# Optimization experiments

Measured on AMD Instinct MI355X. Metric: run time of the kernel, lower is better.

## Reference

```python
import jax, jax.numpy as jnp
import numpy as np

B, T, D, H = 2, 4096, 512, 8
HD = D // H

def setup_inputs() -> dict:
    key = jax.random.key(0)
    ks = jax.random.split(key, 5)
    x = jax.random.normal(ks[0], (B, T, D), dtype=jnp.float32)
    # causal mask: masked_fill where mask == 0
    mask = jnp.tril(jnp.ones((T, T), dtype=jnp.int32))[None, None, :, :]
    qkv_w = jax.random.normal(ks[1], (D, 3 * D), dtype=jnp.float32) * (D ** -0.5)
    qkv_b = jax.random.normal(ks[2], (3 * D,), dtype=jnp.float32) * 0.02
    proj_w = jax.random.normal(ks[3], (D, D), dtype=jnp.float32) * (D ** -0.5)
    proj_b = jax.random.normal(ks[4], (D,), dtype=jnp.float32) * 0.02
    return {"x": x, "mask": mask, "qkv_w": qkv_w, "qkv_b": qkv_b,
            "proj_w": proj_w, "proj_b": proj_b}

def reference(x, mask, qkv_w, qkv_b, proj_w, proj_b):
    b, t, c = x.shape
    qkv = x @ qkv_w + qkv_b                      # [B,T,3D]
    q, k, v = jnp.split(qkv, 3, axis=-1)
    # [B,T,D] -> [B,H,T,hd]
    def heads(a):
        return a.reshape(b, t, H, HD).transpose(0, 2, 1, 3)
    q, k, v = heads(q), heads(k), heads(v)
    att = jnp.einsum('bhqd,bhkd->bhqk', q, k) / (HD ** 0.5)
    att = jnp.where(mask == 0, -jnp.inf, att)
    att = jax.nn.softmax(att, axis=-1)           # dropout p=0.0 -> identity
    out = jnp.einsum('bhqk,bhkd->bhqd', att, v)  # [B,H,T,hd]
    out = out.transpose(0, 2, 1, 3).reshape(b, t, c)
    return out @ proj_w + proj_b
```

## Files before the change

### kernel.cpp

```cpp
#include <hip/hip_runtime.h>
#include <hip/hip_bf16.h>


typedef __attribute__((ext_vector_type(8))) short bf16x8;
typedef __attribute__((ext_vector_type(4))) float f32x4;
typedef __attribute__((ext_vector_type(16))) float f32x16;
typedef __attribute__((ext_vector_type(2))) int i32x2;

#define DEV static __device__ __forceinline__

DEV unsigned short f2bf(float f) {
    union { float f; unsigned u; } a; a.f = f;
    unsigned r = a.u + 0x7FFFu + ((a.u >> 16) & 1u);
    return (unsigned short)(r >> 16);
}

DEV unsigned pack2(float a, float b) {
    unsigned r;
    asm("v_cvt_pk_bf16_f32 %0, %1, %2" : "=v"(r) : "v"(a), "v"(b));
    return r;
}

DEV void glds16(const void* g, void* l) {
    __builtin_amdgcn_global_load_lds(
        (const __attribute__((address_space(1))) void*)g,
        (__attribute__((address_space(3))) void*)l,
        16, 0, 0);
}

DEV f32x4 mfma(bf16x8 a, bf16x8 b, f32x4 c) {
    return __builtin_amdgcn_mfma_f32_16x16x32_bf16(a, b, c, 0, 0, 0);
}

DEV f32x16 mfma32(bf16x8 a, bf16x8 b, f32x16 c) {
    return __builtin_amdgcn_mfma_f32_32x32x16_bf16(a, b, c, 0, 0, 0);
}

DEV void plswap(unsigned& a, unsigned& b) {
#if __has_builtin(__builtin_amdgcn_permlane32_swap)
    i32x2 r = __builtin_amdgcn_permlane32_swap((int)a, (int)b, false, false);
    a = (unsigned)r.x; b = (unsigned)r.y;
#else
    unsigned sa = __shfl_xor(a, 32), sb = __shfl_xor(b, 32);
    bool hi = (threadIdx.x & 32) != 0;
    unsigned na = hi ? sb : a;
    unsigned nb = hi ? b : sa;
    a = na; b = nb;
#endif
}

DEV float xhalf_sum(float x) {
    unsigned a = __float_as_uint(x), b = a;
    plswap(a, b);
    return __uint_as_float(a) + __uint_as_float(b);
}

__global__ __launch_bounds__(256) void k_cast(const float* __restrict__ x,
                                              unsigned short* __restrict__ xb, int n4) {
    for (int i = blockIdx.x * 256 + threadIdx.x; i < n4; i += gridDim.x * 256) {
        float4 v = ((const float4*)x)[i];
        ushort4 o;
        o.x = f2bf(v.x); o.y = f2bf(v.y); o.z = f2bf(v.z); o.w = f2bf(v.w);
        ((ushort4*)xb)[i] = o;
    }
}

__global__ __launch_bounds__(256) void k_tcast2(const float* __restrict__ qkv_w,
                                                unsigned short* __restrict__ wqkvT,
                                                const float* __restrict__ proj_w,
                                                unsigned short* __restrict__ wprojT) {
    __shared__ float t[64][65];
    const int tid = threadIdx.x;
    int id = blockIdx.x;
    const float* src; unsigned short* dst; int R, C, bx, by;
    if (id < 192) { src = qkv_w; dst = wqkvT; R = 512; C = 1536; bx = id % 24; by = id / 24; }
    else { id -= 192; src = proj_w; dst = wprojT; R = 512; C = 512; bx = id & 7; by = id >> 3; }
#pragma unroll
    for (int e = 0; e < 16; ++e) {
        int idx = e * 256 + tid;
        int r = idx >> 6, c = idx & 63;
        t[r][c] = src[(by * 64 + r) * C + bx * 64 + c];
    }
    __syncthreads();
#pragma unroll
    for (int e = 0; e < 16; ++e) {
        int idx = e * 256 + tid;
        int r = idx >> 6, c = idx & 63;
        dst[(bx * 64 + r) * R + by * 64 + c] = f2bf(t[c][r]);
    }
}

__global__ __launch_bounds__(256) void k_gemm_qkv(
    const unsigned short* __restrict__ xb, const unsigned short* __restrict__ wT,
    const float* __restrict__ bias,
    unsigned short* __restrict__ Qb, unsigned short* __restrict__ Kb,
    unsigned short* __restrict__ Vtb)
{
    __shared__ __attribute__((aligned(16))) unsigned short lA[128 * 64];
    __shared__ __attribute__((aligned(16))) unsigned short lB[128 * 64];
    const int tid = threadIdx.x, lane = tid & 63, w = tid >> 6;
    const int qi = lane & 15, g = lane >> 4;
    const int bm = blockIdx.x & 63, bn = blockIdx.x >> 6;
    const int m0 = bm * 128, n0 = bn * 128;
    const int wr = w >> 1, wc = w & 1;
    const int srow = lane >> 3, sch = (lane & 7) ^ srow;
    const int swz = (qi & 7) << 4;
    f32x4 zero = {0.f, 0.f, 0.f, 0.f};
    f32x4 acc[4][4];
#pragma unroll
    for (int i = 0; i < 4; ++i)
#pragma unroll
        for (int j = 0; j < 4; ++j) acc[i][j] = zero;

    for (int kt = 0; kt < 8; ++kt) {
#pragma unroll
        for (int i = 0; i < 4; ++i) {
            int c = w * 4 + i;
            int row = c * 8 + srow;
            glds16(xb + (m0 + row) * 512 + kt * 64 + sch * 8, (char*)lA + c * 1024);
            glds16(wT + (n0 + row) * 512 + kt * 64 + sch * 8, (char*)lB + c * 1024);
        }
        __syncthreads();
#pragma unroll
        for (int k2 = 0; k2 < 2; ++k2) {
            bf16x8 af[4], bfr[4];
#pragma unroll
            for (int i = 0; i < 4; ++i) {
                int ra = wr * 64 + i * 16 + qi;
                af[i] = *(const bf16x8*)((const char*)lA + ra * 128 + ((k2 * 64 + g * 16) ^ swz));
                int rb = wc * 64 + i * 16 + qi;
                bfr[i] = *(const bf16x8*)((const char*)lB + rb * 128 + ((k2 * 64 + g * 16) ^ swz));
            }
#pragma unroll
            for (int mi = 0; mi < 4; ++mi)
#pragma unroll
                for (int ni = 0; ni < 4; ++ni)
                    acc[mi][ni] = mfma(af[mi], bfr[ni], acc[mi][ni]);
        }
        __syncthreads();
    }

    const int comp = n0 >> 9;
#pragma unroll
    for (int mi = 0; mi < 4; ++mi) {
        int mbase = m0 + wr * 64 + mi * 16 + g * 4;
        int b = mbase >> 12, t = mbase & 4095;
#pragma unroll
        for (int ni = 0; ni < 4; ++ni) {
            int n = n0 + wc * 64 + ni * 16 + qi;
            float bn = bias[n];
            int nn = n & 511;
            int h = nn >> 6, d = nn & 63;
            if (comp == 0) {
                unsigned short* dst = Qb + ((b * 8 + h) * 4096 + t) * 64 + d;
#pragma unroll
                for (int r = 0; r < 4; ++r)
                    dst[r * 64] = f2bf((acc[mi][ni][r] + bn) * 0.18033688011112042f);
            } else if (comp == 1) {
                unsigned short* dst = Kb + ((b * 8 + h) * 4096 + t) * 64 + d;
#pragma unroll
                for (int r = 0; r < 4; ++r)
                    dst[r * 64] = f2bf(acc[mi][ni][r] + bn);
            } else {
                ushort4 pk4;
                pk4.x = f2bf(acc[mi][ni][0] + bn);
                pk4.y = f2bf(acc[mi][ni][1] + bn);
                pk4.z = f2bf(acc[mi][ni][2] + bn);
                pk4.w = f2bf(acc[mi][ni][3] + bn);
                *(ushort4*)(Vtb + ((b * 8 + h) * 64 + d) * 4096 + t) = pk4;
            }
        }
    }
}

__global__ __launch_bounds__(512) void k_attn(
    const unsigned short* __restrict__ Qb, const unsigned short* __restrict__ Kb,
    const unsigned short* __restrict__ Vtb, unsigned short* __restrict__ Ob)
{
    __shared__ __attribute__((aligned(16))) char smem[65536];
    const int tid = threadIdx.x, lane = tid & 63, w = tid >> 6;
    const int l31 = lane & 31, l7 = lane & 7, h = lane >> 5;
    const int pr = w >> 1, sub = w & 1;
    const int idx = blockIdx.x;
    const int bh = idx & 15;
    const int p = idx >> 4;
    const unsigned short* Qh = Qb + bh * 4096 * 64;
    const unsigned short* Kh = Kb + bh * 4096 * 64;
    const unsigned short* Vh = Vtb + bh * 4096 * 64;
    const float NEGINF = -__builtin_inff();

    char* myK = smem + pr * 16384;
    char* myV = myK + 8192;

    const int srw = lane >> 3;
    const int sxor = (l7 ^ srw) * 8;
    const int kOffE = (sub * 32 + srw) * 64 + sxor;
    const int vOffE = (sub * 32 + srw) * 4096 + sxor;
    const int ldsO = sub * 4096;

    const int rowbase = l31 * 128;
    int cx[4];
#pragma unroll
    for (int c = 0; c < 4; ++c) cx[c] = ((2 * c + h) ^ l7) * 16;

    const int qrel = (sub << 5) + l31;

    f32x16 z16;
#pragma unroll
    for (int r = 0; r < 16; ++r) z16[r] = 0.f;

    for (int si = 0; si < 2; ++si) {
        const int qt = si ? p : 63 - p;
        const int Tmax = (qt >> 2) + 1;
        const int qrow = qt * 64 + sub * 32 + l31;

        bf16x8 qf[4];
#pragma unroll
        for (int c = 0; c < 4; ++c)
            qf[c] = *(const bf16x8*)(Qh + qrow * 64 + 16 * c + 8 * h);

        f32x16 o0 = z16, o1 = z16;
        float li = 0.f;

        for (int t = 0; t < Tmax; ++t) {
            const int j = 4 * t + pr;
            const bool act = (j <= qt);
            if (act) {
                const unsigned short* kp = Kh + j * 4096 + kOffE;
                const unsigned short* vp = Vh + vOffE + j * 64;
#pragma unroll
                for (int i = 0; i < 4; ++i) {
                    glds16(kp + i * 512,   myK + ldsO + i * 1024);
                    glds16(vp + i * 32768, myV + ldsO + i * 1024);
                }
            }
            __syncthreads();
            if (act) {
                const char* lk = myK;
                const char* lv = myV;
                f32x16 s0, s1;
                __builtin_amdgcn_s_setprio(1);
                {
                    bf16x8 k0 = *(const bf16x8*)(lk + rowbase + cx[0]);
                    bf16x8 k1 = *(const bf16x8*)(lk + 4096 + rowbase + cx[0]);
                    s0 = mfma32(k0, qf[0], z16);
                    s1 = mfma32(k1, qf[0], z16);
                }
#pragma unroll
                for (int c = 1; c < 4; ++c) {
                    bf16x8 k0 = *(const bf16x8*)(lk + rowbase + cx[c]);
                    bf16x8 k1 = *(const bf16x8*)(lk + 4096 + rowbase + cx[c]);
                    s0 = mfma32(k0, qf[c], s0);
                    s1 = mfma32(k1, qf[c], s1);
                }
                __builtin_amdgcn_s_setprio(0);

                if (j == qt) {
#pragma unroll
                    for (int r = 0; r < 16; ++r) {
                        int rr = 4 * h + (r & 3) + 8 * (r >> 2);
                        if (rr > qrel) s0[r] = NEGINF;
                        if (rr + 32 > qrel) s1[r] = NEGINF;
                    }
                }

#pragma unroll
                for (int r = 0; r < 16; ++r) {
                    s0[r] = __builtin_amdgcn_exp2f(s0[r]);
                    s1[r] = __builtin_amdgcn_exp2f(s1[r]);
                }
                float a8[8];
#pragma unroll
                for (int r = 0; r < 8; ++r)
                    a8[r] = (s0[r] + s0[r + 8]) + (s1[r] + s1[r + 8]);
                float b0 = (a8[0] + a8[4]) + (a8[1] + a8[5]);
                float b1 = (a8[2] + a8[6]) + (a8[3] + a8[7]);
                li += xhalf_sum(b0 + b1);

                __builtin_amdgcn_s_setprio(1);
#pragma unroll
                for (int c2 = 0; c2 < 4; ++c2) {
                    unsigned u0w, u1w, u2w, u3w;
                    if (c2 < 2) {
                        const int b0i = 8 * c2;
                        u0w = pack2(s0[b0i + 0], s0[b0i + 1]);
                        u1w = pack2(s0[b0i + 2], s0[b0i + 3]);
                        u2w = pack2(s0[b0i + 4], s0[b0i + 5]);
                        u3w = pack2(s0[b0i + 6], s0[b0i + 7]);
                    } else {
                        const int b0i = 8 * (c2 - 2);
                        u0w = pack2(s1[b0i + 0], s1[b0i + 1]);
                        u1w = pack2(s1[b0i + 2], s1[b0i + 3]);
                        u2w = pack2(s1[b0i + 4], s1[b0i + 5]);
                        u3w = pack2(s1[b0i + 6], s1[b0i + 7]);
                    }
                    plswap(u0w, u2w);
                    plswap(u1w, u3w);
                    union { unsigned u[4]; bf16x8 v; } pf;
                    pf.u[0] = u0w; pf.u[1] = u1w; pf.u[2] = u2w; pf.u[3] = u3w;
                    bf16x8 v0 = *(const bf16x8*)(lv + rowbase + cx[c2]);
                    bf16x8 v1 = *(const bf16x8*)(lv + 4096 + rowbase + cx[c2]);
                    o0 = mfma32(v0, pf.v, o0);
                    o1 = mfma32(v1, pf.v, o1);
                }
                __builtin_amdgcn_s_setprio(0);
            }
            __syncthreads();
        }

        float* fsm = (float*)smem;
        if (pr != 0) {
            float* slot = fsm + ((((pr - 1) << 1) + sub) * 64 + lane) * 36;
#pragma unroll
            for (int r4 = 0; r4 < 4; ++r4) {
                f32x4 v0 = {o0[4 * r4], o0[4 * r4 + 1], o0[4 * r4 + 2], o0[4 * r4 + 3]};
                f32x4 v1 = {o1[4 * r4], o1[4 * r4 + 1], o1[4 * r4 + 2], o1[4 * r4 + 3]};
                *(f32x4*)(slot + 4 * r4) = v0;
                *(f32x4*)(slot + 16 + 4 * r4) = v1;
            }
            slot[32] = li;
        }
        __syncthreads();
        if (pr == 0) {
            float l = li;
#pragma unroll
            for (int i = 0; i < 3; ++i) {
                const float* s = fsm + (((i << 1) + sub) * 64 + lane) * 36;
                l += s[32];
#pragma unroll
                for (int r4 = 0; r4 < 4; ++r4) {
                    f32x4 a = *(const f32x4*)(s + 4 * r4);
                    f32x4 b = *(const f32x4*)(s + 16 + 4 * r4);
#pragma unroll
                    for (int e = 0; e < 4; ++e) {
                        o0[4 * r4 + e] += a[e];
                        o1[4 * r4 + e] += b[e];
                    }
                }
            }
            float inv = 1.f / l;
            unsigned short* orow = Ob + ((bh >> 3) * 4096 + qrow) * 512 + (bh & 7) * 64 + 4 * h;
#pragma unroll
            for (int g2 = 0; g2 < 4; ++g2) {
                union { ushort4 s4; unsigned u[2]; } a;
                a.u[0] = pack2(o0[4 * g2 + 0] * inv, o0[4 * g2 + 1] * inv);
                a.u[1] = pack2(o0[4 * g2 + 2] * inv, o0[4 * g2 + 3] * inv);
                *(ushort4*)(orow + 8 * g2) = a.s4;
                a.u[0] = pack2(o1[4 * g2 + 0] * inv, o1[4 * g2 + 1] * inv);
                a.u[1] = pack2(o1[4 * g2 + 2] * inv, o1[4 * g2 + 3] * inv);
                *(ushort4*)(orow + 32 + 8 * g2) = a.s4;
            }
        }
        __syncthreads();
    }
}

__global__ __launch_bounds__(256) void k_gemm_proj(
    const unsigned short* __restrict__ Ob, const unsigned short* __restrict__ wT,
    const float* __restrict__ bias, float* __restrict__ out)
{
    __shared__ __attribute__((aligned(16))) unsigned short lA[128 * 64];
    __shared__ __attribute__((aligned(16))) unsigned short lB[128 * 64];
    const int tid = threadIdx.x, lane = tid & 63, w = tid >> 6;
    const int qi = lane & 15, g = lane >> 4;
    const int bm = blockIdx.x & 63, bn = blockIdx.x >> 6;
    const int m0 = bm * 128, n0 = bn * 128;
    const int wr = w >> 1, wc = w & 1;
    const int srow = lane >> 3, sch = (lane & 7) ^ srow;
    const int swz = (qi & 7) << 4;
    f32x4 zero = {0.f, 0.f, 0.f, 0.f};
    f32x4 acc[4][4];
#pragma unroll
    for (int i = 0; i < 4; ++i)
#pragma unroll
        for (int j = 0; j < 4; ++j) acc[i][j] = zero;

    for (int kt = 0; kt < 8; ++kt) {
#pragma unroll
        for (int i = 0; i < 4; ++i) {
            int c = w * 4 + i;
            int row = c * 8 + srow;
            glds16(Ob + (m0 + row) * 512 + kt * 64 + sch * 8, (char*)lA + c * 1024);
            glds16(wT + (n0 + row) * 512 + kt * 64 + sch * 8, (char*)lB + c * 1024);
        }
        __syncthreads();
#pragma unroll
        for (int k2 = 0; k2 < 2; ++k2) {
            bf16x8 af[4], bfr[4];
#pragma unroll
            for (int i = 0; i < 4; ++i) {
                int ra = wr * 64 + i * 16 + qi;
                af[i] = *(const bf16x8*)((const char*)lA + ra * 128 + ((k2 * 64 + g * 16) ^ swz));
                int rb = wc * 64 + i * 16 + qi;
                bfr[i] = *(const bf16x8*)((const char*)lB + rb * 128 + ((k2 * 64 + g * 16) ^ swz));
            }
#pragma unroll
            for (int mi = 0; mi < 4; ++mi)
#pragma unroll
                for (int ni = 0; ni < 4; ++ni)
                    acc[mi][ni] = mfma(af[mi], bfr[ni], acc[mi][ni]);
        }
        __syncthreads();
    }

#pragma unroll
    for (int mi = 0; mi < 4; ++mi) {
        int mbase = m0 + wr * 64 + mi * 16 + g * 4;
#pragma unroll
        for (int ni = 0; ni < 4; ++ni) {
            int n = n0 + wc * 64 + ni * 16 + qi;
            float bn = bias[n];
#pragma unroll
            for (int r = 0; r < 4; ++r)
                out[(mbase + r) * 512 + n] = acc[mi][ni][r] + bn;
        }
    }
}

extern "C" void kernel_launch(void* const* d_in, const int* in_sizes, int n_in,
                              void* d_out, int out_size, void* d_ws, size_t ws_size,
                              hipStream_t stream) {
    const float* x      = (const float*)d_in[0];
    const float* qkv_w  = (const float*)d_in[2];
    const float* qkv_b  = (const float*)d_in[3];
    const float* proj_w = (const float*)d_in[4];
    const float* proj_b = (const float*)d_in[5];

    char* ws = (char*)d_ws;
    unsigned short* xb     = (unsigned short*)(ws);
    unsigned short* wqkvT  = (unsigned short*)(ws +  8388608);
    unsigned short* wprojT = (unsigned short*)(ws +  9961472);
    unsigned short* Qb     = (unsigned short*)(ws + 10485760);
    unsigned short* Kb     = (unsigned short*)(ws + 18874368);
    unsigned short* Vtb    = (unsigned short*)(ws + 27262976);
    unsigned short* Ob     = (unsigned short*)(ws + 35651584);
    float* out = (float*)d_out;

    k_cast<<<2048, 256, 0, stream>>>(x, xb, 8192 * 512 / 4);
    k_tcast2<<<256, 256, 0, stream>>>(qkv_w, wqkvT, proj_w, wprojT);
    k_gemm_qkv<<<768, 256, 0, stream>>>(xb, wqkvT, qkv_b, Qb, Kb, Vtb);
    k_attn<<<512, 512, 0, stream>>>(Qb, Kb, Vtb, Ob);
    k_gemm_proj<<<256, 256, 0, stream>>>(Ob, wprojT, proj_b, out);
}
```

Measured before the change: 102.8 us.

## Double-buffer K/V tiles in LDS to prefetch the next tile during compute

Shared memory for the attention kernel doubles to 128KB so each wave pair has two K/V buffers. The next key tile is issued with global_load_lds before the current one is computed, and a partial vmcnt wait lets the loads overlap the MFMA work. The intent is to hide global-to-LDS latency that the single-buffer loop exposed at every barrier. The cost is double the LDS per block, which can limit occupancy to one block per CU, and correctness now depends on hand-written waitcnt and barrier ordering.

```diff
diff --git a/kernel.cpp b/kernel.cpp
--- a/kernel.cpp
+++ b/kernel.cpp
@@ -177,7 +177,7 @@
     const unsigned short* __restrict__ Qb, const unsigned short* __restrict__ Kb,
     const unsigned short* __restrict__ Vtb, unsigned short* __restrict__ Ob)
 {
-    __shared__ __attribute__((aligned(16))) char smem[65536];
+    __shared__ __attribute__((aligned(16))) char smem[131072];
     const int tid = threadIdx.x, lane = tid & 63, w = tid >> 6;
     const int l31 = lane & 31, l7 = lane & 7, h = lane >> 5;
     const int pr = w >> 1, sub = w & 1;
@@ -189,8 +189,9 @@
     const unsigned short* Vh = Vtb + bh * 4096 * 64;
     const float NEGINF = -__builtin_inff();
 
-    char* myK = smem + pr * 16384;
-    char* myV = myK + 8192;
+    char* base = smem + pr * 32768;
+    char* myK0 = base;          char* myV0 = base + 8192;
+    char* myK1 = base + 16384;  char* myV1 = base + 24576;
 
     const int srw = lane >> 3;
     const int sxor = (l7 ^ srw) * 8;
@@ -212,6 +213,7 @@
     for (int si = 0; si < 2; ++si) {
         const int qt = si ? p : 63 - p;
         const int Tmax = (qt >> 2) + 1;
+        const int myT = (qt >= pr) ? ((qt - pr) >> 2) + 1 : 0;
         const int qrow = qt * 64 + sub * 32 + l31;
 
         bf16x8 qf[4];
@@ -222,22 +224,42 @@
         f32x16 o0 = z16, o1 = z16;
         float li = 0.f;
 
+        if (myT > 0) {
+            const unsigned short* kp = Kh + pr * 4096 + kOffE;
+            const unsigned short* vp = Vh + vOffE + pr * 64;
+#pragma unroll
+            for (int i = 0; i < 4; ++i) {
+                glds16(kp + i * 512,   myK0 + ldsO + i * 1024);
+                glds16(vp + i * 32768, myV0 + ldsO + i * 1024);
+            }
+        }
+
         for (int t = 0; t < Tmax; ++t) {
-            const int j = 4 * t + pr;
-            const bool act = (j <= qt);
+            const int cur = t & 1;
+            const bool act  = t < myT;
+            const bool actn = (t + 1) < myT;
+            if (actn) {
+                const int jn = 4 * (t + 1) + pr;
+                const unsigned short* kp = Kh + jn * 4096 + kOffE;
+                const unsigned short* vp = Vh + vOffE + jn * 64;
+                char* kd = cur ? myK0 : myK1;
+                char* vd = cur ? myV0 : myV1;
+#pragma unroll
+                for (int i = 0; i < 4; ++i) {
+                    glds16(kp + i * 512,   kd + ldsO + i * 1024);
+                    glds16(vp + i * 32768, vd + ldsO + i * 1024);
+                }
+                asm volatile("s_waitcnt vmcnt(8)" ::: "memory");
+            } else {
+                asm volatile("s_waitcnt vmcnt(0)" ::: "memory");
+            }
+            __builtin_amdgcn_s_barrier();
+            __builtin_amdgcn_sched_barrier(0);
+
             if (act) {
-                const unsigned short* kp = Kh + j * 4096 + kOffE;
-                const unsigned short* vp = Vh + vOffE + j * 64;
-#pragma unroll
-                for (int i = 0; i < 4; ++i) {
-                    glds16(kp + i * 512,   myK + ldsO + i * 1024);
-                    glds16(vp + i * 32768, myV + ldsO + i * 1024);
-                }
-            }
-            __syncthreads();
-            if (act) {
-                const char* lk = myK;
-                const char* lv = myV;
+                const int j = 4 * t + pr;
+                const char* lk = cur ? myK1 : myK0;
+                const char* lv = cur ? myV1 : myV0;
                 f32x16 s0, s1;
                 __builtin_amdgcn_s_setprio(1);
                 {
@@ -305,7 +327,8 @@
                 }
                 __builtin_amdgcn_s_setprio(0);
             }
-            __syncthreads();
+            __builtin_amdgcn_s_barrier();
+            __builtin_amdgcn_sched_barrier(0);
         }
 
         float* fsm = (float*)smem;
```

Result: slower. 114.3 us (+11.1%).
